# Optimization experiments

Measured on AMD Instinct MI355X. Metric: run time of the kernel, lower is better.

## Reference

```python
import jax, jax.numpy as jnp
import numpy as np

B, S, DIM = 1, 2048, 4096
NH, NKV, HD = 32, 8, 128
REPEATS = NH // NKV
ROPE_THETA = 10000.0


def setup_inputs() -> dict:
    key = jax.random.key(0)
    ks = jax.random.split(key, 6)
    x = jax.random.normal(ks[0], (B, S, DIM), jnp.float32) * 0.02
    wq = jax.random.normal(ks[1], (NH * HD, DIM), jnp.float32) * 0.02
    wk = jax.random.normal(ks[2], (NKV * HD, DIM), jnp.float32) * 0.02
    wv = jax.random.normal(ks[3], (NKV * HD, DIM), jnp.float32) * 0.02
    wo = jax.random.normal(ks[4], (DIM, NH * HD), jnp.float32) * 0.02
    # rotary frequencies (real cos/sin form of complex freqs_cis)
    inv_freq = 1.0 / (ROPE_THETA ** (jnp.arange(0, HD, 2, dtype=jnp.float32) / HD))
    ang = jnp.arange(S, dtype=jnp.float32)[:, None] * inv_freq[None, :]  # [S, HD//2]
    freqs_cos = jnp.cos(ang)
    freqs_sin = jnp.sin(ang)
    positions = jnp.arange(S, dtype=jnp.int32)  # prompt phase: all positions
    # additive causal mask
    mask = jnp.where(jnp.tril(jnp.ones((S, S), bool)), 0.0, -1e9).astype(jnp.float32)
    cache_k = jnp.zeros((B, S, NKV, HD), jnp.float32)
    cache_v = jnp.zeros((B, S, NKV, HD), jnp.float32)
    return dict(x=x, wq=wq, wk=wk, wv=wv, wo=wo, freqs_cos=freqs_cos,
                freqs_sin=freqs_sin, cache_k=cache_k, cache_v=cache_v,
                positions=positions, mask=mask)


def apply_rope(t, cos, sin):
    # t: [b, s, h, d]; pairs are (d0,d1),(d2,d3),... matching view_as_complex
    tr = t[..., 0::2]
    ti = t[..., 1::2]
    c = cos[None, :, None, :]
    s = sin[None, :, None, :]
    out_r = tr * c - ti * s
    out_i = tr * s + ti * c
    return jnp.stack([out_r, out_i], axis=-1).reshape(t.shape)


def reference(x, wq, wk, wv, wo, freqs_cos, freqs_sin, cache_k, cache_v, positions, mask):
    b, s, _ = x.shape
    xq = jnp.einsum('bsd,od->bso', x, wq).reshape(b, s, NH, HD)
    xk = jnp.einsum('bsd,od->bso', x, wk).reshape(b, s, NKV, HD)
    xv = jnp.einsum('bsd,od->bso', x, wv).reshape(b, s, NKV, HD)
    xq = apply_rope(xq, freqs_cos, freqs_sin)
    xk = apply_rope(xk, freqs_cos, freqs_sin)
    # KV-cache scatter (prompt phase writes; output uses fresh xk/xv here)
    cache_k = cache_k.at[:, positions].set(xk)
    cache_v = cache_v.at[:, positions].set(xv)
    # GQA: repeat_interleave kv heads to match query heads
    k = jnp.repeat(xk, REPEATS, axis=2).transpose(0, 2, 1, 3)  # [b, NH, s, HD]
    v = jnp.repeat(xv, REPEATS, axis=2).transpose(0, 2, 1, 3)
    q = xq.transpose(0, 2, 1, 3)
    scale = HD ** -0.5
    scores = jnp.einsum('bhqd,bhkd->bhqk', q, k) * scale + mask[None, None]
    probs = jax.nn.softmax(scores.astype(jnp.float32), axis=-1).astype(q.dtype)
    out = jnp.einsum('bhqk,bhkd->bhqd', probs, v)
    out = out.transpose(0, 2, 1, 3).reshape(b, s, NH * HD)
    return jnp.einsum('bso,do->bsd', out, wo)
```

## Files before the change

### kernel.cpp

```cpp
#include <hip/hip_runtime.h>
#include <hip/hip_bf16.h>
#include <stdint.h>

typedef __bf16 bf16_t;
typedef __attribute__((ext_vector_type(8))) __bf16 bf16x8;
typedef __attribute__((ext_vector_type(4))) float f32x4;
typedef __attribute__((ext_vector_type(8))) unsigned short u16x8;

#define S_LEN 2048
#define DIM   4096
#define QKVN  6144
#define NHEAD 32
#define HDIM  128

typedef __attribute__((address_space(1))) unsigned int as1_u32;
typedef __attribute__((address_space(3))) unsigned int as3_u32;

__device__ __forceinline__ unsigned short f2bf(float f) {
  unsigned u = __builtin_bit_cast(unsigned, f);
  u += 0x7fffu + ((u >> 16) & 1u);
  return (unsigned short)(u >> 16);
}

__device__ __forceinline__ void gload_lds16(const void* g, void* l) {
  __builtin_amdgcn_global_load_lds(
      (as1_u32*)(unsigned long long)(uintptr_t)g,
      (as3_u32*)(unsigned int)(uintptr_t)l,
      16, 0, 0);
}

__global__ __launch_bounds__(256) void cvt_kernel(const float* __restrict__ in,
                                                  unsigned short* __restrict__ out,
                                                  int n4) {
  int idx = blockIdx.x * 256 + threadIdx.x;
  int stride = gridDim.x * 256;
  for (int i = idx; i < n4; i += stride) {
    float4 v = ((const float4*)in)[i];
    ushort4 o;
    o.x = f2bf(v.x); o.y = f2bf(v.y); o.z = f2bf(v.z); o.w = f2bf(v.w);
    ((ushort4*)out)[i] = o;
  }
}

__device__ __forceinline__ void stage_A(const bf16_t* __restrict__ g, int ldk,
                                        long rowBase, int k0, char* ldsBase, int tid) {
#pragma unroll
  for (int i = 0; i < 2; ++i) {
    int c = tid + i * 512;
    int row = c >> 2, slot = c & 3;
    const bf16_t* src = g + (rowBase + row) * (long)ldk + k0
                        + ((slot ^ ((row >> 1) & 3)) << 3);
    gload_lds16(src, ldsBase + c * 16);
  }
}

__device__ __forceinline__ void stage_B(const bf16_t* __restrict__ g, int ldk,
                                        long rowBase, int k0, char* ldsBase, int tid) {
  int row = tid >> 2, slot = tid & 3;
  const bf16_t* src = g + (rowBase + row) * (long)ldk + k0
                      + ((slot ^ ((row >> 1) & 3)) << 3);
  gload_lds16(src, ldsBase + tid * 16);
}

__device__ __forceinline__ bf16x8 frag_ld(const char* base, int row, int lg) {
  return *(const bf16x8*)(base + row * 64 + ((lg ^ ((row >> 1) & 3)) << 4));
}

template <int OUTF32>
__global__ __launch_bounds__(512, 2) void gemm256(const bf16_t* __restrict__ A,
                                                  const bf16_t* __restrict__ B,
                                                  void* __restrict__ Cout,
                                                  int M, int N, int K, int nxt) {
  __shared__ char lds[49152];
  const int tid = threadIdx.x;
  const int lane = tid & 63, w = tid >> 6;
  const int wm = w >> 1, wn = w & 1;
  const int lg = lane >> 4, lr = lane & 15;
  const int nwg = gridDim.x;
  const int orig = blockIdx.x;
  const int wgid = (orig & 7) * (nwg >> 3) + (orig >> 3);
  const int bx = wgid % nxt, by = wgid / nxt;
  const long rowA = (long)by * 256;
  const long rowB = (long)bx * 128;

  f32x4 acc[4][4];
  const f32x4 z4 = {0.f, 0.f, 0.f, 0.f};
#pragma unroll
  for (int i = 0; i < 4; ++i)
#pragma unroll
    for (int j = 0; j < 4; ++j) acc[i][j] = z4;

  stage_A(A, K, rowA, 0, lds, tid);
  stage_B(B, K, rowB, 0, lds + 16384, tid);
  stage_A(A, K, rowA, 32, lds + 24576, tid);
  stage_B(B, K, rowB, 32, lds + 40960, tid);
  asm volatile("s_waitcnt vmcnt(3)" ::: "memory");
  __builtin_amdgcn_s_barrier();

  const int nt = K >> 5;
  for (int t = 0; t < nt; ++t) {
    char* Ab = lds + (t & 1) * 24576;
    char* Bb = Ab + 16384;
    bf16x8 af[4], bfr[4];
#pragma unroll
    for (int mf = 0; mf < 4; ++mf) af[mf] = frag_ld(Ab, wm * 64 + mf * 16 + lr, lg);
#pragma unroll
    for (int nf = 0; nf < 4; ++nf) bfr[nf] = frag_ld(Bb, wn * 64 + nf * 16 + lr, lg);
    asm volatile("s_waitcnt lgkmcnt(0)" ::: "memory");
    __builtin_amdgcn_sched_barrier(0);
    __builtin_amdgcn_s_barrier();
    if (t + 2 < nt) {
      stage_A(A, K, rowA, (t + 2) * 32, Ab, tid);
      stage_B(B, K, rowB, (t + 2) * 32, Bb, tid);
    }
    __builtin_amdgcn_s_setprio(1);
#pragma unroll
    for (int mf = 0; mf < 4; ++mf)
#pragma unroll
      for (int nf = 0; nf < 4; ++nf)
        acc[mf][nf] = __builtin_amdgcn_mfma_f32_16x16x32_bf16(af[mf], bfr[nf],
                                                              acc[mf][nf], 0, 0, 0);
    __builtin_amdgcn_s_setprio(0);
    if (t + 2 < nt) {
      asm volatile("s_waitcnt vmcnt(3)" ::: "memory");
    } else {
      asm volatile("s_waitcnt vmcnt(0)" ::: "memory");
    }
    __builtin_amdgcn_s_barrier();
  }

  const long crow = rowA + wm * 64;
  const long ccol = rowB + wn * 64;
  if (OUTF32) {
    float* C = (float*)Cout;
#pragma unroll
    for (int mf = 0; mf < 4; ++mf)
#pragma unroll
      for (int j = 0; j < 4; ++j) {
        long row = crow + mf * 16 + lg * 4 + j;
        float* cp = C + row * N + ccol + lr;
#pragma unroll
        for (int nf = 0; nf < 4; ++nf) cp[nf * 16] = acc[mf][nf][j];
      }
  } else {
    unsigned short* C = (unsigned short*)Cout;
#pragma unroll
    for (int mf = 0; mf < 4; ++mf)
#pragma unroll
      for (int j = 0; j < 4; ++j) {
        long row = crow + mf * 16 + lg * 4 + j;
        unsigned short* cp = C + row * N + ccol + lr;
#pragma unroll
        for (int nf = 0; nf < 4; ++nf) cp[nf * 16] = f2bf(acc[mf][nf][j]);
      }
  }
}

__global__ __launch_bounds__(256) void rope_kernel(unsigned int* __restrict__ qkv32,
                                                   const float* __restrict__ cosb,
                                                   const float* __restrict__ sinb) {
  int t = blockIdx.x * 256 + threadIdx.x;
  int i  = t & 63;
  int sh = t >> 6;
  int hh = sh % 40;
  int s  = sh / 40;
  int col2 = (hh < 32) ? (hh * 64 + i) : (2048 + (hh - 32) * 64 + i);
  unsigned int* p = qkv32 + (long)s * (QKVN / 2) + col2;
  unsigned int v = *p;
  float tr = __builtin_bit_cast(float, (v & 0xffffu) << 16);
  float ti = __builtin_bit_cast(float, v & 0xffff0000u);
  float c  = cosb[s * 64 + i];
  float sn = sinb[s * 64 + i];
  float orr = tr * c - ti * sn;
  float oi  = tr * sn + ti * c;
  *p = (unsigned int)f2bf(orr) | ((unsigned int)f2bf(oi) << 16);
}

__global__ __launch_bounds__(256) void vtrans_kernel(const bf16_t* __restrict__ qkv,
                                                     bf16_t* __restrict__ vT) {
  const int kh = blockIdx.x;
  const int hd = threadIdx.x & 127;
  const int s0 = blockIdx.y * 16 + (threadIdx.x >> 7) * 8;
  u16x8 v;
#pragma unroll
  for (int e = 0; e < 8; ++e)
    v[e] = *(const unsigned short*)(qkv + (long)(s0 + e) * QKVN + 5120 + kh * HDIM + hd);
  *(u16x8*)(vT + ((long)kh * HDIM + hd) * S_LEN + s0) = v;
}

__global__ __launch_bounds__(256) void attn_kernel(const bf16_t* __restrict__ qkv,
                                                   const bf16_t* __restrict__ vT,
                                                   unsigned short* __restrict__ ob) {
  __shared__ bf16_t Kt[64 * 128];
  __shared__ bf16_t Vt[128 * 64];
  __shared__ bf16_t Pl[4 * 16 * 64];
  const int h  = blockIdx.x;
  const int qi = 31 - blockIdx.y;
  const int qb = qi * 64;
  const int kh = h >> 2;
  const int tid = threadIdx.x, lane = tid & 63, w = tid >> 6;
  const int lg = lane >> 4, lr = lane & 15;
  const int qrow0 = qb + w * 16;

  bf16x8 qf[4];
  const bf16_t* qptr = qkv + (long)(qrow0 + lr) * QKVN + h * HDIM + lg * 8;
#pragma unroll
  for (int kk = 0; kk < 4; ++kk) qf[kk] = *(const bf16x8*)(qptr + kk * 32);

  const f32x4 z4 = {0.f, 0.f, 0.f, 0.f};
  f32x4 oacc[8];
#pragma unroll
  for (int c = 0; c < 8; ++c) oacc[c] = z4;
  float m[4]    = {-1e30f, -1e30f, -1e30f, -1e30f};
  float lsum[4] = {0.f, 0.f, 0.f, 0.f};

  char* KtB = (char*)Kt;
  char* VtB = (char*)Vt;
  char* PlB = (char*)Pl + w * 2048;
  const float scale = 0.08838834764831845f;
  const int ntiles = qi + 1;

  for (int t = 0; t < ntiles; ++t) {
    const int kv0 = t * 64;
    __syncthreads();
#pragma unroll
    for (int it = 0; it < 4; ++it) {
      int cch = tid + it * 256;
      int r = cch >> 4, c = cch & 15;
      const bf16_t* src = qkv + (long)(kv0 + r) * QKVN + 4096 + kh * HDIM
                          + ((c ^ (r & 7)) * 8);
      gload_lds16(src, KtB + cch * 16);
    }
#pragma unroll
    for (int it = 0; it < 4; ++it) {
      int cch = tid + it * 256;
      int hd = cch >> 3, c = cch & 7;
      const bf16_t* src = vT + ((long)kh * HDIM + hd) * S_LEN + kv0
                          + ((c ^ (hd & 7)) * 8);
      gload_lds16(src, VtB + cch * 16);
    }
    __syncthreads();

    f32x4 sf[4];
#pragma unroll
    for (int f = 0; f < 4; ++f) {
      f32x4 a = z4;
      int n = f * 16 + lr;
      int rb = n * 256, sw = (n & 7) << 4;
#pragma unroll
      for (int kk = 0; kk < 4; ++kk) {
        bf16x8 kf = *(const bf16x8*)(KtB + rb + (((kk * 4 + lg) * 16) ^ sw));
        a = __builtin_amdgcn_mfma_f32_16x16x32_bf16(qf[kk], kf, a, 0, 0, 0);
      }
      sf[f] = a;
    }

    float sc_arr[4];
#pragma unroll
    for (int j = 0; j < 4; ++j) {
      int qrow = qrow0 + lg * 4 + j;
      float sv[4];
#pragma unroll
      for (int f = 0; f < 4; ++f) {
        float s = sf[f][j] * scale;
        if (kv0 + f * 16 + lr > qrow) s = -1e9f;
        sv[f] = s;
      }
      float mx = fmaxf(fmaxf(sv[0], sv[1]), fmaxf(sv[2], sv[3]));
      mx = fmaxf(mx, __shfl_xor(mx, 1));
      mx = fmaxf(mx, __shfl_xor(mx, 2));
      mx = fmaxf(mx, __shfl_xor(mx, 4));
      mx = fmaxf(mx, __shfl_xor(mx, 8));
      float mn = fmaxf(m[j], mx);
      float p[4];
#pragma unroll
      for (int f = 0; f < 4; ++f) p[f] = __expf(sv[f] - mn);
      float ps = (p[0] + p[1]) + (p[2] + p[3]);
      ps += __shfl_xor(ps, 1);
      ps += __shfl_xor(ps, 2);
      ps += __shfl_xor(ps, 4);
      ps += __shfl_xor(ps, 8);
      float sc = __expf(m[j] - mn);
      lsum[j] = lsum[j] * sc + ps;
      m[j] = mn;
      sc_arr[j] = sc;
      int row = lg * 4 + j;
      int swp = (row & 7) << 4;
#pragma unroll
      for (int f = 0; f < 4; ++f)
        *(unsigned short*)(PlB + row * 128 + (((f * 16 + lr) * 2) ^ swp)) = f2bf(p[f]);
    }
#pragma unroll
    for (int c = 0; c < 8; ++c)
#pragma unroll
      for (int j = 0; j < 4; ++j) oacc[c][j] *= sc_arr[j];

    bf16x8 pfr[2];
#pragma unroll
    for (int kk = 0; kk < 2; ++kk)
      pfr[kk] = *(const bf16x8*)(PlB + lr * 128 + (((kk * 4 + lg) * 16) ^ ((lr & 7) << 4)));
#pragma unroll
    for (int c = 0; c < 8; ++c) {
      int hd = c * 16 + lr;
      int rb = hd * 128, sw = (hd & 7) << 4;
#pragma unroll
      for (int kk = 0; kk < 2; ++kk) {
        bf16x8 vf = *(const bf16x8*)(VtB + rb + (((kk * 4 + lg) * 16) ^ sw));
        oacc[c] = __builtin_amdgcn_mfma_f32_16x16x32_bf16(pfr[kk], vf, oacc[c], 0, 0, 0);
      }
    }
  }

  float rl[4];
#pragma unroll
  for (int j = 0; j < 4; ++j) rl[j] = 1.f / lsum[j];
#pragma unroll
  for (int c = 0; c < 8; ++c)
#pragma unroll
    for (int j = 0; j < 4; ++j) {
      long row = qrow0 + lg * 4 + j;
      ob[row * 4096 + h * 128 + c * 16 + lr] = f2bf(oacc[c][j] * rl[j]);
    }
}

extern "C" void kernel_launch(void* const* d_in, const int* in_sizes, int n_in,
                              void* d_out, int out_size, void* d_ws, size_t ws_size,
                              hipStream_t stream) {
  const float* x  = (const float*)d_in[0];
  const float* wq = (const float*)d_in[1];
  const float* wk = (const float*)d_in[2];
  const float* wv = (const float*)d_in[3];
  const float* wo = (const float*)d_in[4];
  const float* fc = (const float*)d_in[5];
  const float* fs = (const float*)d_in[6];

  char* ws = (char*)d_ws;
  bf16_t* xb    = (bf16_t*)(ws + 0);
  bf16_t* wqkvb = (bf16_t*)(ws + 16777216);
  bf16_t* wob   = (bf16_t*)(ws + 67108864);
  bf16_t* qkv   = (bf16_t*)(ws + 100663296);
  bf16_t* ob    = (bf16_t*)(ws + 125829120);
  bf16_t* vT    = (bf16_t*)(ws + 0);

  cvt_kernel<<<2048, 256, 0, stream>>>(x,  (unsigned short*)xb,                    (2048 * 4096) / 4);
  cvt_kernel<<<2048, 256, 0, stream>>>(wq, (unsigned short*)wqkvb,                 (4096 * 4096) / 4);
  cvt_kernel<<<1024, 256, 0, stream>>>(wk, (unsigned short*)(wqkvb + 4096 * 4096), (1024 * 4096) / 4);
  cvt_kernel<<<1024, 256, 0, stream>>>(wv, (unsigned short*)(wqkvb + 5120 * 4096), (1024 * 4096) / 4);
  cvt_kernel<<<2048, 256, 0, stream>>>(wo, (unsigned short*)wob,                   (4096 * 4096) / 4);

  gemm256<0><<<384, 512, 0, stream>>>(xb, wqkvb, qkv, 2048, 6144, 4096, 48);
  vtrans_kernel<<<dim3(8, 128), 256, 0, stream>>>(qkv, vT);
  rope_kernel<<<20480, 256, 0, stream>>>((unsigned int*)qkv, fc, fs);
  attn_kernel<<<dim3(32, 32), 256, 0, stream>>>(qkv, vT, (unsigned short*)ob);
  gemm256<1><<<256, 512, 0, stream>>>(ob, wob, d_out, 2048, 4096, 4096, 32);
}
```

Baseline: 362.3 us.

## Replace 256x128 GEMM with 128x128 triple-buffered register-prefetch pipeline

The GEMM moves from 512-thread 256x128 tiles with double-buffered LDS to 256-thread 128x128 tiles with three LDS slots. Fragments for the next k-step are loaded into a second register set while the current MFMAs run, and global loads are issued three steps ahead. This is meant to hide LDS and global latency behind MFMA work and to double the number of workgroups. In exchange each tile gets less reuse per LDS byte, since the A tile is halved, and register pressure rises from the two fragment sets.

```diff
diff --git a/kernel.cpp b/kernel.cpp
--- a/kernel.cpp
+++ b/kernel.cpp
@@ -42,35 +42,41 @@
   }
 }
 
-__device__ __forceinline__ void stage_A(const bf16_t* __restrict__ g, int ldk,
-                                        long rowBase, int k0, char* ldsBase, int tid) {
-#pragma unroll
-  for (int i = 0; i < 2; ++i) {
-    int c = tid + i * 512;
-    int row = c >> 2, slot = c & 3;
-    const bf16_t* src = g + (rowBase + row) * (long)ldk + k0
-                        + ((slot ^ ((row >> 1) & 3)) << 3);
-    gload_lds16(src, ldsBase + c * 16);
-  }
-}
-
-__device__ __forceinline__ void stage_B(const bf16_t* __restrict__ g, int ldk,
-                                        long rowBase, int k0, char* ldsBase, int tid) {
-  int row = tid >> 2, slot = tid & 3;
-  const bf16_t* src = g + (rowBase + row) * (long)ldk + k0
-                      + ((slot ^ ((row >> 1) & 3)) << 3);
-  gload_lds16(src, ldsBase + tid * 16);
-}
-
 __device__ __forceinline__ bf16x8 frag_ld(const char* base, int row, int lg) {
   return *(const bf16x8*)(base + row * 64 + ((lg ^ ((row >> 1) & 3)) << 4));
 }
 
+__device__ __forceinline__ void load_frags(const char* slot, int wm, int wn,
+                                           int lg, int lr, bf16x8* af, bf16x8* bf) {
+#pragma unroll
+  for (int i = 0; i < 4; ++i) af[i] = frag_ld(slot, wm * 64 + i * 16 + lr, lg);
+#pragma unroll
+  for (int i = 0; i < 4; ++i) bf[i] = frag_ld(slot + 8192, wn * 64 + i * 16 + lr, lg);
+}
+
+__device__ __forceinline__ void stage_slot(const bf16_t* a0, const bf16_t* b0,
+                                           long ldk64, int k0, char* slot, int tid) {
+  gload_lds16(a0 + k0,         slot + tid * 16);
+  gload_lds16(a0 + ldk64 + k0, slot + 4096 + tid * 16);
+  gload_lds16(b0 + k0,         slot + 8192 + tid * 16);
+  gload_lds16(b0 + ldk64 + k0, slot + 12288 + tid * 16);
+}
+
+__device__ __forceinline__ void mfma16(const bf16x8* af, const bf16x8* bf,
+                                       f32x4 (*acc)[4]) {
+#pragma unroll
+  for (int mf = 0; mf < 4; ++mf)
+#pragma unroll
+    for (int nf = 0; nf < 4; ++nf)
+      acc[mf][nf] = __builtin_amdgcn_mfma_f32_16x16x32_bf16(af[mf], bf[nf],
+                                                            acc[mf][nf], 0, 0, 0);
+}
+
 template <int OUTF32>
-__global__ __launch_bounds__(512, 2) void gemm256(const bf16_t* __restrict__ A,
-                                                  const bf16_t* __restrict__ B,
-                                                  void* __restrict__ Cout,
-                                                  int M, int N, int K, int nxt) {
+__global__ __launch_bounds__(256, 2) void gemm_pipe(const bf16_t* __restrict__ A,
+                                                    const bf16_t* __restrict__ B,
+                                                    void* __restrict__ Cout,
+                                                    int M, int N, int K, int nxt) {
   __shared__ char lds[49152];
   const int tid = threadIdx.x;
   const int lane = tid & 63, w = tid >> 6;
@@ -80,7 +86,7 @@
   const int orig = blockIdx.x;
   const int wgid = (orig & 7) * (nwg >> 3) + (orig >> 3);
   const int bx = wgid % nxt, by = wgid / nxt;
-  const long rowA = (long)by * 256;
+  const long rowA = (long)by * 128;
   const long rowB = (long)bx * 128;
 
   f32x4 acc[4][4];
@@ -90,44 +96,54 @@
 #pragma unroll
     for (int j = 0; j < 4; ++j) acc[i][j] = z4;
 
-  stage_A(A, K, rowA, 0, lds, tid);
-  stage_B(B, K, rowB, 0, lds + 16384, tid);
-  stage_A(A, K, rowA, 32, lds + 24576, tid);
-  stage_B(B, K, rowB, 32, lds + 40960, tid);
-  asm volatile("s_waitcnt vmcnt(3)" ::: "memory");
+  const int srow = tid >> 2, s4 = tid & 3;
+  const long ldk64 = (long)64 * K;
+  const bf16_t* Asrc = A + (rowA + srow) * (long)K + ((s4 ^ ((srow >> 1) & 3)) << 3);
+  const bf16_t* Bsrc = B + (rowB + srow) * (long)K + ((s4 ^ ((srow >> 1) & 3)) << 3);
+
+  char* p0 = lds;
+  char* p1 = lds + 16384;
+  char* p2 = lds + 32768;
+  const int nt = K >> 5;
+
+  bf16x8 afA[4], bfA[4], afB[4], bfB[4];
+
+  stage_slot(Asrc, Bsrc, ldk64, 0,  p0, tid);
+  stage_slot(Asrc, Bsrc, ldk64, 32, p1, tid);
+  stage_slot(Asrc, Bsrc, ldk64, 64, p2, tid);
+  asm volatile("s_waitcnt vmcnt(8)" ::: "memory");
   __builtin_amdgcn_s_barrier();
-
-  const int nt = K >> 5;
-  for (int t = 0; t < nt; ++t) {
-    char* Ab = lds + (t & 1) * 24576;
-    char* Bb = Ab + 16384;
-    bf16x8 af[4], bfr[4];
-#pragma unroll
-    for (int mf = 0; mf < 4; ++mf) af[mf] = frag_ld(Ab, wm * 64 + mf * 16 + lr, lg);
-#pragma unroll
-    for (int nf = 0; nf < 4; ++nf) bfr[nf] = frag_ld(Bb, wn * 64 + nf * 16 + lr, lg);
-    asm volatile("s_waitcnt lgkmcnt(0)" ::: "memory");
-    __builtin_amdgcn_sched_barrier(0);
-    __builtin_amdgcn_s_barrier();
-    if (t + 2 < nt) {
-      stage_A(A, K, rowA, (t + 2) * 32, Ab, tid);
-      stage_B(B, K, rowB, (t + 2) * 32, Bb, tid);
-    }
-    __builtin_amdgcn_s_setprio(1);
-#pragma unroll
-    for (int mf = 0; mf < 4; ++mf)
-#pragma unroll
-      for (int nf = 0; nf < 4; ++nf)
-        acc[mf][nf] = __builtin_amdgcn_mfma_f32_16x16x32_bf16(af[mf], bfr[nf],
-                                                              acc[mf][nf], 0, 0, 0);
-    __builtin_amdgcn_s_setprio(0);
-    if (t + 2 < nt) {
-      asm volatile("s_waitcnt vmcnt(3)" ::: "memory");
-    } else {
-      asm volatile("s_waitcnt vmcnt(0)" ::: "memory");
-    }
-    __builtin_amdgcn_s_barrier();
-  }
+  load_frags(p0, wm, wn, lg, lr, afA, bfA);
+  asm volatile("s_waitcnt lgkmcnt(0)" ::: "memory");
+  __builtin_amdgcn_sched_barrier(0);
+  asm volatile("s_waitcnt vmcnt(4)" ::: "memory");
+  __builtin_amdgcn_s_barrier();
+
+#define GSTEP(T, afC, bfC, afN, bfN, SR, SW)                                 \
+  {                                                                          \
+    load_frags(SR, wm, wn, lg, lr, afN, bfN);                                \
+    if ((T) + 3 < nt) stage_slot(Asrc, Bsrc, ldk64, ((T) + 3) * 32, SW, tid);\
+    __builtin_amdgcn_s_setprio(1);                                           \
+    mfma16(afC, bfC, acc);                                                   \
+    __builtin_amdgcn_s_setprio(0);                                           \
+    asm volatile("s_waitcnt lgkmcnt(0)" ::: "memory");                       \
+    __builtin_amdgcn_sched_barrier(0);                                       \
+    if ((T) + 3 < nt) { asm volatile("s_waitcnt vmcnt(4)" ::: "memory"); }   \
+    else              { asm volatile("s_waitcnt vmcnt(0)" ::: "memory"); }   \
+    __builtin_amdgcn_s_barrier();                                            \
+  }
+
+  int t = 0;
+  for (; t < nt - 2; t += 2) {
+    GSTEP(t,     afA, bfA, afB, bfB, p1, p0);
+    GSTEP(t + 1, afB, bfB, afA, bfA, p2, p1);
+    char* tmp = p2; p2 = p1; p1 = p0; p0 = tmp;
+  }
+  GSTEP(t, afA, bfA, afB, bfB, p1, p0);
+  __builtin_amdgcn_s_setprio(1);
+  mfma16(afB, bfB, acc);
+  __builtin_amdgcn_s_setprio(0);
+#undef GSTEP
 
   const long crow = rowA + wm * 64;
   const long ccol = rowB + wn * 64;
@@ -348,9 +364,9 @@
   cvt_kernel<<<1024, 256, 0, stream>>>(wv, (unsigned short*)(wqkvb + 5120 * 4096), (1024 * 4096) / 4);
   cvt_kernel<<<2048, 256, 0, stream>>>(wo, (unsigned short*)wob,                   (4096 * 4096) / 4);
 
-  gemm256<0><<<384, 512, 0, stream>>>(xb, wqkvb, qkv, 2048, 6144, 4096, 48);
+  gemm_pipe<0><<<768, 256, 0, stream>>>(xb, wqkvb, qkv, 2048, 6144, 4096, 48);
   vtrans_kernel<<<dim3(8, 128), 256, 0, stream>>>(qkv, vT);
   rope_kernel<<<20480, 256, 0, stream>>>((unsigned int*)qkv, fc, fs);
   attn_kernel<<<dim3(32, 32), 256, 0, stream>>>(qkv, vT, (unsigned short*)ob);
-  gemm256<1><<<256, 512, 0, stream>>>(ob, wob, d_out, 2048, 4096, 4096, 32);
-}
+  gemm_pipe<1><<<512, 256, 0, stream>>>(ob, wob, d_out, 2048, 4096, 4096, 32);
+}
```

Result: slower. 374.2 us (+3.3%).

## Enlarge attention query tile to 128 rows and merge fp32-to-bf16 conversions

Applied to the files above, without the earlier changes.

Attention blocks now cover 128 query rows with 8 waves (512 threads), so each K/V tile staged in LDS is shared by twice as many query rows and the grid shrinks to 32x16. Waves whose rows lie entirely before the current KV tile skip its compute, which handles the extra causal tile. The five separate fp32-to-bf16 conversion launches become one fused launch to cut launch overhead. The larger blocks add load imbalance across waves and fewer blocks for the scheduler to balance.

```diff
diff --git a/kernel.cpp b/kernel.cpp
--- a/kernel.cpp
+++ b/kernel.cpp
@@ -29,16 +29,32 @@
       16, 0, 0);
 }
 
-__global__ __launch_bounds__(256) void cvt_kernel(const float* __restrict__ in,
-                                                  unsigned short* __restrict__ out,
-                                                  int n4) {
-  int idx = blockIdx.x * 256 + threadIdx.x;
-  int stride = gridDim.x * 256;
-  for (int i = idx; i < n4; i += stride) {
-    float4 v = ((const float4*)in)[i];
-    ushort4 o;
-    o.x = f2bf(v.x); o.y = f2bf(v.y); o.z = f2bf(v.z); o.w = f2bf(v.w);
-    ((ushort4*)out)[i] = o;
+__global__ __launch_bounds__(256) void cvt5_kernel(const float* __restrict__ x,
+                                                   const float* __restrict__ wq,
+                                                   const float* __restrict__ wk,
+                                                   const float* __restrict__ wv,
+                                                   const float* __restrict__ wo,
+                                                   ushort4* __restrict__ xb,
+                                                   ushort4* __restrict__ wqkvb,
+                                                   ushort4* __restrict__ wob) {
+  const long N0 = 2097152;
+  const long N1 = N0 + 4194304;
+  const long N2 = N1 + 1048576;
+  const long N3 = N2 + 1048576;
+  const long N4 = N3 + 4194304;
+  long idx = (long)blockIdx.x * 256 + threadIdx.x;
+  long stride = (long)gridDim.x * 256;
+  for (long i = idx; i < N4; i += stride) {
+    const float4* s; ushort4* d; long o;
+    if (i < N0)      { s = (const float4*)x;  d = xb;              o = i; }
+    else if (i < N1) { s = (const float4*)wq; d = wqkvb;           o = i - N0; }
+    else if (i < N2) { s = (const float4*)wk; d = wqkvb + 4194304; o = i - N1; }
+    else if (i < N3) { s = (const float4*)wv; d = wqkvb + 5242880; o = i - N2; }
+    else             { s = (const float4*)wo; d = wob;             o = i - N3; }
+    float4 v = s[o];
+    ushort4 r;
+    r.x = f2bf(v.x); r.y = f2bf(v.y); r.z = f2bf(v.z); r.w = f2bf(v.w);
+    d[o] = r;
   }
 }
 
@@ -188,15 +204,15 @@
   *(u16x8*)(vT + ((long)kh * HDIM + hd) * S_LEN + s0) = v;
 }
 
-__global__ __launch_bounds__(256) void attn_kernel(const bf16_t* __restrict__ qkv,
+__global__ __launch_bounds__(512) void attn_kernel(const bf16_t* __restrict__ qkv,
                                                    const bf16_t* __restrict__ vT,
                                                    unsigned short* __restrict__ ob) {
   __shared__ bf16_t Kt[64 * 128];
   __shared__ bf16_t Vt[128 * 64];
-  __shared__ bf16_t Pl[4 * 16 * 64];
+  __shared__ bf16_t Pl[8 * 16 * 64];
   const int h  = blockIdx.x;
-  const int qi = 31 - blockIdx.y;
-  const int qb = qi * 64;
+  const int qi = 15 - (int)blockIdx.y;
+  const int qb = qi * 128;
   const int kh = h >> 2;
   const int tid = threadIdx.x, lane = tid & 63, w = tid >> 6;
   const int lg = lane >> 4, lr = lane & 15;
@@ -218,28 +234,30 @@
   char* VtB = (char*)Vt;
   char* PlB = (char*)Pl + w * 2048;
   const float scale = 0.08838834764831845f;
-  const int ntiles = qi + 1;
+  const int ntiles = 2 * qi + 2;
+  const int wqmax = qrow0 + 15;
 
   for (int t = 0; t < ntiles; ++t) {
     const int kv0 = t * 64;
     __syncthreads();
 #pragma unroll
-    for (int it = 0; it < 4; ++it) {
-      int cch = tid + it * 256;
+    for (int it = 0; it < 2; ++it) {
+      int cch = tid + it * 512;
       int r = cch >> 4, c = cch & 15;
       const bf16_t* src = qkv + (long)(kv0 + r) * QKVN + 4096 + kh * HDIM
                           + ((c ^ (r & 7)) * 8);
       gload_lds16(src, KtB + cch * 16);
     }
 #pragma unroll
-    for (int it = 0; it < 4; ++it) {
-      int cch = tid + it * 256;
+    for (int it = 0; it < 2; ++it) {
+      int cch = tid + it * 512;
       int hd = cch >> 3, c = cch & 7;
       const bf16_t* src = vT + ((long)kh * HDIM + hd) * S_LEN + kv0
                           + ((c ^ (hd & 7)) * 8);
       gload_lds16(src, VtB + cch * 16);
     }
     __syncthreads();
+    if (kv0 > wqmax) continue;
 
     f32x4 sf[4];
 #pragma unroll
@@ -342,15 +360,12 @@
   bf16_t* ob    = (bf16_t*)(ws + 125829120);
   bf16_t* vT    = (bf16_t*)(ws + 0);
 
-  cvt_kernel<<<2048, 256, 0, stream>>>(x,  (unsigned short*)xb,                    (2048 * 4096) / 4);
-  cvt_kernel<<<2048, 256, 0, stream>>>(wq, (unsigned short*)wqkvb,                 (4096 * 4096) / 4);
-  cvt_kernel<<<1024, 256, 0, stream>>>(wk, (unsigned short*)(wqkvb + 4096 * 4096), (1024 * 4096) / 4);
-  cvt_kernel<<<1024, 256, 0, stream>>>(wv, (unsigned short*)(wqkvb + 5120 * 4096), (1024 * 4096) / 4);
-  cvt_kernel<<<2048, 256, 0, stream>>>(wo, (unsigned short*)wob,                   (4096 * 4096) / 4);
+  cvt5_kernel<<<2048, 256, 0, stream>>>(x, wq, wk, wv, wo,
+                                        (ushort4*)xb, (ushort4*)wqkvb, (ushort4*)wob);
 
   gemm256<0><<<384, 512, 0, stream>>>(xb, wqkvb, qkv, 2048, 6144, 4096, 48);
   vtrans_kernel<<<dim3(8, 128), 256, 0, stream>>>(qkv, vT);
   rope_kernel<<<20480, 256, 0, stream>>>((unsigned int*)qkv, fc, fs);
-  attn_kernel<<<dim3(32, 32), 256, 0, stream>>>(qkv, vT, (unsigned short*)ob);
+  attn_kernel<<<dim3(32, 16), 512, 0, stream>>>(qkv, vT, (unsigned short*)ob);
   gemm256<1><<<256, 512, 0, stream>>>(ob, wob, d_out, 2048, 4096, 4096, 32);
 }
```

After: 354.4 us. 1.02x faster.
